# Performance work log

Hardware: AMD Instinct MI355X
Metric: run time of the kernel (lower is better)

The kernel has to match this reference:

```python
import jax, jax.numpy as jnp
import numpy as np

T = 200000  # stack depth
V = 130     # vocab_size == input_dim
H = 512     # hid_dim
L = 2       # n_layers


def setup_inputs() -> dict:
    key = jax.random.key(0)
    ks = jax.random.split(key, 24)
    s = 0.05
    inp = {
        "input": jax.random.normal(ks[0], (1, 1, V), jnp.float32),
        "prev_Val": jax.random.normal(ks[1], (T, V), jnp.float32),
        "prev_stg": jax.random.uniform(ks[2], (T,), jnp.float32),
        "prev_read": jax.random.normal(ks[3], (V,), jnp.float32),
        "prev_h": jax.random.normal(ks[4], (L, 1, H), jnp.float32) * 0.1,
        "prev_c": jax.random.normal(ks[5], (L, 1, H), jnp.float32) * 0.1,
        # LSTM layer 0 (pytorch layout: W_ih (4H, in), W_hh (4H, H), gates i,f,g,o)
        "W_ih0": jax.random.normal(ks[6], (4 * H, V), jnp.float32) * s,
        "W_hh0": jax.random.normal(ks[7], (4 * H, H), jnp.float32) * s,
        "b_ih0": jax.random.normal(ks[8], (4 * H,), jnp.float32) * s,
        "b_hh0": jax.random.normal(ks[9], (4 * H,), jnp.float32) * s,
        # LSTM layer 1
        "W_ih1": jax.random.normal(ks[10], (4 * H, H), jnp.float32) * s,
        "W_hh1": jax.random.normal(ks[11], (4 * H, H), jnp.float32) * s,
        "b_ih1": jax.random.normal(ks[12], (4 * H,), jnp.float32) * s,
        "b_hh1": jax.random.normal(ks[13], (4 * H,), jnp.float32) * s,
        # gate heads (original inits these to zeros; random here to exercise math)
        "Wd": jax.random.normal(ks[14], (H,), jnp.float32) * s,
        "Bd": jax.random.normal(ks[15], (), jnp.float32) * s,
        "Wu": jax.random.normal(ks[16], (H,), jnp.float32) * s,
        "Bu": jax.random.normal(ks[17], (), jnp.float32) * s,
        "Wv": jax.random.normal(ks[18], (H, V), jnp.float32) * s,
        "Bv": jax.random.normal(ks[19], (V,), jnp.float32) * s,
        "Wo": jax.random.normal(ks[20], (H, H), jnp.float32) * s,
        "Bo": jax.random.normal(ks[21], (H,), jnp.float32) * s,
    }
    return inp


def _lstm_cell(x, h, c, Wih, Whh, bih, bhh):
    # x: (1, in), h/c: (1, H)
    g = x @ Wih.T + h @ Whh.T + bih + bhh  # (1, 4H)
    i, f, gg, o = jnp.split(g, 4, axis=-1)
    c2 = jax.nn.sigmoid(f) * c + jax.nn.sigmoid(i) * jnp.tanh(gg)
    h2 = jax.nn.sigmoid(o) * jnp.tanh(c2)
    return h2, c2


def reference(input, prev_Val, prev_stg, prev_read, prev_h, prev_c,
              W_ih0, W_hh0, b_ih0, b_hh0, W_ih1, W_hh1, b_ih1, b_hh1,
              Wd, Bd, Wu, Bu, Wv, Bv, Wo, Bo):
    x = (input + prev_read)[0]  # (1, V), seq_len == 1, batch == 1
    h1, c1 = _lstm_cell(x, prev_h[0], prev_c[0], W_ih0, W_hh0, b_ih0, b_hh0)
    h2, c2 = _lstm_cell(h1, prev_h[1], prev_c[1], W_ih1, W_hh1, b_ih1, b_hh1)
    output = h2  # (1, H)

    dt = jax.nn.sigmoid(output @ Wd + Bd)[0]      # scalar push strength
    ut = jax.nn.sigmoid(output @ Wu + Bu)[0]      # scalar pop strength
    vt = jnp.tanh(output @ Wv + Bv)               # (1, V) pushed value
    ot = jnp.tanh(output @ Wo + Bo)               # (1, H) controller output

    Val = jnp.concatenate([prev_Val, vt], axis=0)  # (T+1, V)

    # pop pass (top -> bottom): stg[i] = max(0, prev_stg[i] - max(0, ut)); ut -= stg[i]
    def pop_step(u, s):
        sn = jnp.maximum(0.0, s - jnp.maximum(0.0, u))
        return u - sn, sn
    _, stg_popped = jax.lax.scan(pop_step, ut, prev_stg, reverse=True)
    stg = jnp.concatenate([stg_popped, dt[None]])  # (T+1,)

    # read pass (top -> bottom): coef = min(stg[i], max(0, read)); read -= stg[i]
    def read_step(r, s):
        coef = jnp.minimum(s, jnp.maximum(0.0, r))
        return r - s, coef
    _, coefs = jax.lax.scan(read_step, jnp.asarray(1.0, stg.dtype), stg, reverse=True)
    rt = coefs @ Val  # (V,)

    h_new = jnp.stack([h1, h2])  # (L, 1, H)
    c_new = jnp.stack([c1, c2])
    return ot, Val, stg, rt, h_new, c_new
```

## Files before the change

kernel.cpp:

```cpp
#include <hip/hip_runtime.h>

#define T_DEPTH 200000
#define V_DIM   130
#define H_DIM   512

#define OT_OFF   0
#define VAL_OFF  512
#define STG_OFF  26000642
#define RT_OFF   26200643
#define HN_OFF   26200773
#define CN_OFF   26201797

#define NV4 6500000
#define NS2 100000
#define A1  1625000
#define A2  3250000
#define A3  4875000
#define MVB 128
#define CPB 1536

typedef float f32x4 __attribute__((ext_vector_type(4)));
typedef float f32x2 __attribute__((ext_vector_type(2)));

static __device__ __forceinline__ float sigmoidf_(float x) {
  return 1.0f / (1.0f + expf(-x));
}

static __device__ __forceinline__ void copy_val4(const f32x4* __restrict__ vin,
                                                 f32x4* __restrict__ vout,
                                                 int lo, int hi, int w, int S) {
  int u = lo + w;
  for (; u + 3 * S < hi; u += 4 * S) {
    f32x4 a = __builtin_nontemporal_load(vin + u);
    f32x4 b = __builtin_nontemporal_load(vin + u + S);
    f32x4 c = __builtin_nontemporal_load(vin + u + 2 * S);
    f32x4 d = __builtin_nontemporal_load(vin + u + 3 * S);
    __builtin_nontemporal_store(a, vout + u);
    __builtin_nontemporal_store(b, vout + u + S);
    __builtin_nontemporal_store(c, vout + u + 2 * S);
    __builtin_nontemporal_store(d, vout + u + 3 * S);
  }
  for (; u < hi; u += S) {
    f32x4 a = __builtin_nontemporal_load(vin + u);
    __builtin_nontemporal_store(a, vout + u);
  }
}

static __device__ __forceinline__ void lstm_unit(
    const float* __restrict__ Wih, int in_dim,
    const float* __restrict__ x_a, const float* __restrict__ x_b,
    const float* __restrict__ Whh, const float* __restrict__ hprev,
    const float* __restrict__ bih, const float* __restrict__ bhh,
    const float* __restrict__ cprev, int j, int lane,
    float* __restrict__ h_out, float* __restrict__ c_out) {
  float pg[4];
#pragma unroll
  for (int q = 0; q < 4; ++q) {
    int row = q * H_DIM + j;
    const float* wr = Wih + row * in_dim;
    const float* wh = Whh + row * H_DIM;
    float acc = 0.f;
    if (x_b) {
      for (int c = lane; c < in_dim; c += 64) acc += wr[c] * (x_a[c] + x_b[c]);
    } else {
      for (int c = lane; c < in_dim; c += 64) acc += wr[c] * x_a[c];
    }
    for (int k = lane; k < H_DIM; k += 64) acc += wh[k] * hprev[k];
    for (int off = 32; off; off >>= 1) acc += __shfl_down(acc, off, 64);
    pg[q] = acc;
  }
  if (lane == 0) {
    float ig = sigmoidf_(pg[0] + bih[j] + bhh[j]);
    float fg = sigmoidf_(pg[1] + bih[H_DIM + j] + bhh[H_DIM + j]);
    float gg = tanhf(pg[2] + bih[2 * H_DIM + j] + bhh[2 * H_DIM + j]);
    float og = sigmoidf_(pg[3] + bih[3 * H_DIM + j] + bhh[3 * H_DIM + j]);
    float cn = fg * cprev[j] + ig * gg;
    float hn = og * tanhf(cn);
    h_out[j] = hn;
    c_out[j] = cn;
  }
}

__global__ void k1_l0(const float* __restrict__ Wih, const float* __restrict__ Whh,
                      const float* __restrict__ bih, const float* __restrict__ bhh,
                      const float* __restrict__ inp, const float* __restrict__ prd,
                      const float* __restrict__ hprev, const float* __restrict__ cprev,
                      const f32x4* __restrict__ vin, const f32x2* __restrict__ sin2,
                      float* __restrict__ out) {
  int bid = blockIdx.x, tid = threadIdx.x;
  if (bid < MVB) {
    lstm_unit(Wih, V_DIM, inp, prd, Whh, hprev, bih, bhh, cprev,
              bid * 4 + (tid >> 6), tid & 63, out + HN_OFF, out + CN_OFF);
  } else {
    int w = (bid - MVB) * 256 + tid;
    int S = (gridDim.x - MVB) * 256;
    f32x2* __restrict__ sout = reinterpret_cast<f32x2*>(out + STG_OFF);
    for (int u = w; u < NS2; u += S) {
      f32x2 sv = __builtin_nontemporal_load(sin2 + u);
      __builtin_nontemporal_store(sv, sout + u);
    }
    copy_val4(vin, reinterpret_cast<f32x4*>(out + VAL_OFF), 0, A1, w, S);
  }
}

__global__ void k2_l1(const float* __restrict__ Wih, const float* __restrict__ Whh,
                      const float* __restrict__ bih, const float* __restrict__ bhh,
                      const float* __restrict__ hprev, const float* __restrict__ cprev,
                      const f32x4* __restrict__ vin, float* __restrict__ out) {
  int bid = blockIdx.x, tid = threadIdx.x;
  if (bid < MVB) {
    lstm_unit(Wih, H_DIM, out + HN_OFF, nullptr, Whh, hprev, bih, bhh, cprev,
              bid * 4 + (tid >> 6), tid & 63,
              out + HN_OFF + H_DIM, out + CN_OFF + H_DIM);
  } else {
    int w = (bid - MVB) * 256 + tid;
    int S = (gridDim.x - MVB) * 256;
    copy_val4(vin, reinterpret_cast<f32x4*>(out + VAL_OFF), A1, A2, w, S);
  }
}

__global__ void k3_heads(const float* __restrict__ Wv, const float* __restrict__ Bv,
                         const float* __restrict__ Wo, const float* __restrict__ Bo,
                         const float* __restrict__ Wd, const float* __restrict__ Bd,
                         const float* __restrict__ Wu, const float* __restrict__ Bu,
                         const f32x4* __restrict__ vin, float* __restrict__ ws,
                         float* __restrict__ out) {
  int bid = blockIdx.x, tid = threadIdx.x;
  const float* h2 = out + HN_OFF + H_DIM;
  if (bid < 2) {
    int t = bid * 256 + tid;
    float a0 = 0.f, a1 = 0.f, a2 = 0.f, a3 = 0.f;
    for (int k = 0; k < H_DIM; k += 4) {
      a0 += h2[k]     * Wo[k * H_DIM + t];
      a1 += h2[k + 1] * Wo[(k + 1) * H_DIM + t];
      a2 += h2[k + 2] * Wo[(k + 2) * H_DIM + t];
      a3 += h2[k + 3] * Wo[(k + 3) * H_DIM + t];
    }
    out[OT_OFF + t] = tanhf(((a0 + a1) + (a2 + a3)) + Bo[t]);
  } else if (bid == 2) {
    if (tid < V_DIM) {
      float a0 = 0.f, a1 = 0.f, a2 = 0.f, a3 = 0.f;
      for (int k = 0; k < H_DIM; k += 4) {
        a0 += h2[k]     * Wv[k * V_DIM + tid];
        a1 += h2[k + 1] * Wv[(k + 1) * V_DIM + tid];
        a2 += h2[k + 2] * Wv[(k + 2) * V_DIM + tid];
        a3 += h2[k + 3] * Wv[(k + 3) * V_DIM + tid];
      }
      out[VAL_OFF + T_DEPTH * V_DIM + tid] = tanhf(((a0 + a1) + (a2 + a3)) + Bv[tid]);
    }
  } else if (bid == 3) {
    int wid = tid >> 6, lane = tid & 63;
    if (wid < 2) {
      const float* wv = (wid == 0) ? Wd : Wu;
      float acc = 0.f;
      for (int k = lane; k < H_DIM; k += 64) acc += h2[k] * wv[k];
      for (int off = 32; off; off >>= 1) acc += __shfl_down(acc, off, 64);
      if (lane == 0) {
        if (wid == 0) {
          float dt = sigmoidf_(acc + Bd[0]);
          ws[0] = dt;
          out[STG_OFF + T_DEPTH] = dt;
        } else {
          ws[1] = sigmoidf_(acc + Bu[0]);
        }
      }
    }
  } else {
    int w = (bid - 4) * 256 + tid;
    int S = (gridDim.x - 4) * 256;
    copy_val4(vin, reinterpret_cast<f32x4*>(out + VAL_OFF), A2, A3, w, S);
  }
}

__global__ void k4_top(const float* __restrict__ prev_stg, const float* __restrict__ prev_val,
                       const float* __restrict__ ws, const f32x4* __restrict__ vin,
                       float* __restrict__ out) {
  int bid = blockIdx.x, t = threadIdx.x;
  if (bid == 0) {
    float dt = ws[0];
    float u  = ws[1];
    float r  = 1.0f;
    float acc = 0.f;
    {
      float coef = fminf(dt, fmaxf(0.f, r));
      if (t < V_DIM) acc += coef * out[VAL_OFF + T_DEPTH * V_DIM + t];
      r -= dt;
    }
    for (int i = T_DEPTH - 1; i >= 0; --i) {
      bool pop_active = (u > 0.f);
      if (!pop_active && r <= 0.f) break;
      float s  = prev_stg[i];
      float sn = fmaxf(0.f, s - fmaxf(0.f, u));
      u -= sn;
      if (pop_active && t == 0) out[STG_OFF + i] = sn;
      float coef = fminf(sn, fmaxf(0.f, r));
      r -= sn;
      if (coef > 0.f && t < V_DIM) acc += coef * prev_val[i * V_DIM + t];
    }
    if (t < V_DIM) out[RT_OFF + t] = acc;
  } else {
    int w = (bid - 1) * 256 + t;
    int S = (gridDim.x - 1) * 256;
    copy_val4(vin, reinterpret_cast<f32x4*>(out + VAL_OFF), A3, NV4, w, S);
  }
}

extern "C" void kernel_launch(void* const* d_in, const int* in_sizes, int n_in,
                              void* d_out, int out_size, void* d_ws, size_t ws_size,
                              hipStream_t stream) {
  (void)in_sizes; (void)n_in; (void)out_size; (void)ws_size;
  const float* input     = (const float*)d_in[0];
  const float* prev_Val  = (const float*)d_in[1];
  const float* prev_stg  = (const float*)d_in[2];
  const float* prev_read = (const float*)d_in[3];
  const float* prev_h    = (const float*)d_in[4];
  const float* prev_c    = (const float*)d_in[5];
  const float* W_ih0 = (const float*)d_in[6];
  const float* W_hh0 = (const float*)d_in[7];
  const float* b_ih0 = (const float*)d_in[8];
  const float* b_hh0 = (const float*)d_in[9];
  const float* W_ih1 = (const float*)d_in[10];
  const float* W_hh1 = (const float*)d_in[11];
  const float* b_ih1 = (const float*)d_in[12];
  const float* b_hh1 = (const float*)d_in[13];
  const float* Wd = (const float*)d_in[14];
  const float* Bd = (const float*)d_in[15];
  const float* Wu = (const float*)d_in[16];
  const float* Bu = (const float*)d_in[17];
  const float* Wv = (const float*)d_in[18];
  const float* Bv = (const float*)d_in[19];
  const float* Wo = (const float*)d_in[20];
  const float* Bo = (const float*)d_in[21];

  float* out = (float*)d_out;
  float* ws  = (float*)d_ws;

  const f32x4* vin = (const f32x4*)prev_Val;
  const f32x2* sin2 = (const f32x2*)prev_stg;

  k1_l0<<<MVB + CPB, 256, 0, stream>>>(W_ih0, W_hh0, b_ih0, b_hh0, input, prev_read,
                                       prev_h, prev_c, vin, sin2, out);
  k2_l1<<<MVB + CPB, 256, 0, stream>>>(W_ih1, W_hh1, b_ih1, b_hh1,
                                       prev_h + H_DIM, prev_c + H_DIM, vin, out);
  k3_heads<<<4 + CPB, 256, 0, stream>>>(Wv, Bv, Wo, Bo, Wd, Bd, Wu, Bu, vin, ws, out);
  k4_top<<<1 + CPB, 256, 0, stream>>>(prev_stg, prev_Val, ws, vin, out);
}
```

Before: 297.2 us.

## Split bulk Val/stg copy into separate kernel ahead of serial LSTM chain

The large Val/stg copy is no longer spread across four kernels alongside the LSTM, head and stack work. It now runs as one dedicated grid-stride kernel with plain (temporal) loads and stores, followed by small LSTM, head and stack-pass kernels. Intermediate h and c now go to workspace instead of being read back from the output buffer. This removes the interleaving of the serial compute chain with the copy, but the small kernels no longer overlap with the copy, and the nontemporal hints are dropped.

```diff
diff --git a/kernel.cpp b/kernel.cpp
--- a/kernel.cpp
+++ b/kernel.cpp
@@ -11,38 +11,29 @@
 #define HN_OFF   26200773
 #define CN_OFF   26201797
 
+#define WS_DTUT  0
+#define WS_H1    64
+#define WS_C1    576
+#define WS_H2    1088
+#define WS_C2    1600
+
 #define NV4 6500000
 #define NS2 100000
-#define A1  1625000
-#define A2  3250000
-#define A3  4875000
-#define MVB 128
-#define CPB 1536
-
-typedef float f32x4 __attribute__((ext_vector_type(4)));
-typedef float f32x2 __attribute__((ext_vector_type(2)));
 
 static __device__ __forceinline__ float sigmoidf_(float x) {
   return 1.0f / (1.0f + expf(-x));
 }
 
-static __device__ __forceinline__ void copy_val4(const f32x4* __restrict__ vin,
-                                                 f32x4* __restrict__ vout,
-                                                 int lo, int hi, int w, int S) {
-  int u = lo + w;
-  for (; u + 3 * S < hi; u += 4 * S) {
-    f32x4 a = __builtin_nontemporal_load(vin + u);
-    f32x4 b = __builtin_nontemporal_load(vin + u + S);
-    f32x4 c = __builtin_nontemporal_load(vin + u + 2 * S);
-    f32x4 d = __builtin_nontemporal_load(vin + u + 3 * S);
-    __builtin_nontemporal_store(a, vout + u);
-    __builtin_nontemporal_store(b, vout + u + S);
-    __builtin_nontemporal_store(c, vout + u + 2 * S);
-    __builtin_nontemporal_store(d, vout + u + 3 * S);
-  }
-  for (; u < hi; u += S) {
-    f32x4 a = __builtin_nontemporal_load(vin + u);
-    __builtin_nontemporal_store(a, vout + u);
+__global__ void k_bulk(const float4* __restrict__ val_in,
+                       const float2* __restrict__ stg_in,
+                       float* __restrict__ out) {
+  const int NT = NV4 + NS2;
+  float4* __restrict__ val_out = reinterpret_cast<float4*>(out + VAL_OFF);
+  float2* __restrict__ stg_out = reinterpret_cast<float2*>(out + STG_OFF);
+  int stride = gridDim.x * blockDim.x;
+  for (int u = blockIdx.x * blockDim.x + threadIdx.x; u < NT; u += stride) {
+    if (u < NV4) val_out[u] = val_in[u];
+    else { int s = u - NV4; stg_out[s] = stg_in[s]; }
   }
 }
 
@@ -52,6 +43,7 @@
     const float* __restrict__ Whh, const float* __restrict__ hprev,
     const float* __restrict__ bih, const float* __restrict__ bhh,
     const float* __restrict__ cprev, int j, int lane,
+    float* __restrict__ h_ws, float* __restrict__ c_ws,
     float* __restrict__ h_out, float* __restrict__ c_out) {
   float pg[4];
 #pragma unroll
@@ -76,57 +68,37 @@
     float og = sigmoidf_(pg[3] + bih[3 * H_DIM + j] + bhh[3 * H_DIM + j]);
     float cn = fg * cprev[j] + ig * gg;
     float hn = og * tanhf(cn);
-    h_out[j] = hn;
-    c_out[j] = cn;
-  }
-}
-
-__global__ void k1_l0(const float* __restrict__ Wih, const float* __restrict__ Whh,
-                      const float* __restrict__ bih, const float* __restrict__ bhh,
-                      const float* __restrict__ inp, const float* __restrict__ prd,
-                      const float* __restrict__ hprev, const float* __restrict__ cprev,
-                      const f32x4* __restrict__ vin, const f32x2* __restrict__ sin2,
-                      float* __restrict__ out) {
+    h_ws[j] = hn; c_ws[j] = cn;
+    h_out[j] = hn; c_out[j] = cn;
+  }
+}
+
+__global__ void kL0(const float* __restrict__ Wih, const float* __restrict__ Whh,
+                    const float* __restrict__ bih, const float* __restrict__ bhh,
+                    const float* __restrict__ inp, const float* __restrict__ prd,
+                    const float* __restrict__ hprev, const float* __restrict__ cprev,
+                    float* __restrict__ ws, float* __restrict__ out) {
+  int j = blockIdx.x * 4 + (threadIdx.x >> 6), lane = threadIdx.x & 63;
+  lstm_unit(Wih, V_DIM, inp, prd, Whh, hprev, bih, bhh, cprev, j, lane,
+            ws + WS_H1, ws + WS_C1, out + HN_OFF, out + CN_OFF);
+}
+
+__global__ void kL1(const float* __restrict__ Wih, const float* __restrict__ Whh,
+                    const float* __restrict__ bih, const float* __restrict__ bhh,
+                    const float* __restrict__ hprev, const float* __restrict__ cprev,
+                    float* __restrict__ ws, float* __restrict__ out) {
+  int j = blockIdx.x * 4 + (threadIdx.x >> 6), lane = threadIdx.x & 63;
+  lstm_unit(Wih, H_DIM, ws + WS_H1, nullptr, Whh, hprev, bih, bhh, cprev, j, lane,
+            ws + WS_H2, ws + WS_C2, out + HN_OFF + H_DIM, out + CN_OFF + H_DIM);
+}
+
+__global__ void kheads(const float* __restrict__ Wv, const float* __restrict__ Bv,
+                       const float* __restrict__ Wo, const float* __restrict__ Bo,
+                       const float* __restrict__ Wd, const float* __restrict__ Bd,
+                       const float* __restrict__ Wu, const float* __restrict__ Bu,
+                       float* __restrict__ ws, float* __restrict__ out) {
   int bid = blockIdx.x, tid = threadIdx.x;
-  if (bid < MVB) {
-    lstm_unit(Wih, V_DIM, inp, prd, Whh, hprev, bih, bhh, cprev,
-              bid * 4 + (tid >> 6), tid & 63, out + HN_OFF, out + CN_OFF);
-  } else {
-    int w = (bid - MVB) * 256 + tid;
-    int S = (gridDim.x - MVB) * 256;
-    f32x2* __restrict__ sout = reinterpret_cast<f32x2*>(out + STG_OFF);
-    for (int u = w; u < NS2; u += S) {
-      f32x2 sv = __builtin_nontemporal_load(sin2 + u);
-      __builtin_nontemporal_store(sv, sout + u);
-    }
-    copy_val4(vin, reinterpret_cast<f32x4*>(out + VAL_OFF), 0, A1, w, S);
-  }
-}
-
-__global__ void k2_l1(const float* __restrict__ Wih, const float* __restrict__ Whh,
-                      const float* __restrict__ bih, const float* __restrict__ bhh,
-                      const float* __restrict__ hprev, const float* __restrict__ cprev,
-                      const f32x4* __restrict__ vin, float* __restrict__ out) {
-  int bid = blockIdx.x, tid = threadIdx.x;
-  if (bid < MVB) {
-    lstm_unit(Wih, H_DIM, out + HN_OFF, nullptr, Whh, hprev, bih, bhh, cprev,
-              bid * 4 + (tid >> 6), tid & 63,
-              out + HN_OFF + H_DIM, out + CN_OFF + H_DIM);
-  } else {
-    int w = (bid - MVB) * 256 + tid;
-    int S = (gridDim.x - MVB) * 256;
-    copy_val4(vin, reinterpret_cast<f32x4*>(out + VAL_OFF), A1, A2, w, S);
-  }
-}
-
-__global__ void k3_heads(const float* __restrict__ Wv, const float* __restrict__ Bv,
-                         const float* __restrict__ Wo, const float* __restrict__ Bo,
-                         const float* __restrict__ Wd, const float* __restrict__ Bd,
-                         const float* __restrict__ Wu, const float* __restrict__ Bu,
-                         const f32x4* __restrict__ vin, float* __restrict__ ws,
-                         float* __restrict__ out) {
-  int bid = blockIdx.x, tid = threadIdx.x;
-  const float* h2 = out + HN_OFF + H_DIM;
+  const float* h2 = ws + WS_H2;
   if (bid < 2) {
     int t = bid * 256 + tid;
     float a0 = 0.f, a1 = 0.f, a2 = 0.f, a3 = 0.f;
@@ -148,7 +120,7 @@
       }
       out[VAL_OFF + T_DEPTH * V_DIM + tid] = tanhf(((a0 + a1) + (a2 + a3)) + Bv[tid]);
     }
-  } else if (bid == 3) {
+  } else {
     int wid = tid >> 6, lane = tid & 63;
     if (wid < 2) {
       const float* wv = (wid == 0) ? Wd : Wu;
@@ -158,51 +130,40 @@
       if (lane == 0) {
         if (wid == 0) {
           float dt = sigmoidf_(acc + Bd[0]);
-          ws[0] = dt;
+          ws[WS_DTUT + 0] = dt;
           out[STG_OFF + T_DEPTH] = dt;
         } else {
-          ws[1] = sigmoidf_(acc + Bu[0]);
+          ws[WS_DTUT + 1] = sigmoidf_(acc + Bu[0]);
         }
       }
     }
-  } else {
-    int w = (bid - 4) * 256 + tid;
-    int S = (gridDim.x - 4) * 256;
-    copy_val4(vin, reinterpret_cast<f32x4*>(out + VAL_OFF), A2, A3, w, S);
-  }
-}
-
-__global__ void k4_top(const float* __restrict__ prev_stg, const float* __restrict__ prev_val,
-                       const float* __restrict__ ws, const f32x4* __restrict__ vin,
-                       float* __restrict__ out) {
-  int bid = blockIdx.x, t = threadIdx.x;
-  if (bid == 0) {
-    float dt = ws[0];
-    float u  = ws[1];
-    float r  = 1.0f;
-    float acc = 0.f;
-    {
-      float coef = fminf(dt, fmaxf(0.f, r));
-      if (t < V_DIM) acc += coef * out[VAL_OFF + T_DEPTH * V_DIM + t];
-      r -= dt;
-    }
-    for (int i = T_DEPTH - 1; i >= 0; --i) {
-      bool pop_active = (u > 0.f);
-      if (!pop_active && r <= 0.f) break;
-      float s  = prev_stg[i];
-      float sn = fmaxf(0.f, s - fmaxf(0.f, u));
-      u -= sn;
-      if (pop_active && t == 0) out[STG_OFF + i] = sn;
-      float coef = fminf(sn, fmaxf(0.f, r));
-      r -= sn;
-      if (coef > 0.f && t < V_DIM) acc += coef * prev_val[i * V_DIM + t];
-    }
-    if (t < V_DIM) out[RT_OFF + t] = acc;
-  } else {
-    int w = (bid - 1) * 256 + t;
-    int S = (gridDim.x - 1) * 256;
-    copy_val4(vin, reinterpret_cast<f32x4*>(out + VAL_OFF), A3, NV4, w, S);
-  }
+  }
+}
+
+__global__ void ktop(const float* __restrict__ prev_stg, const float* __restrict__ prev_val,
+                     const float* __restrict__ ws, float* __restrict__ out) {
+  int t = threadIdx.x;
+  float dt = ws[WS_DTUT + 0];
+  float u  = ws[WS_DTUT + 1];
+  float r  = 1.0f;
+  float acc = 0.f;
+  {
+    float coef = fminf(dt, fmaxf(0.f, r));
+    if (t < V_DIM) acc += coef * out[VAL_OFF + T_DEPTH * V_DIM + t];
+    r -= dt;
+  }
+  for (int i = T_DEPTH - 1; i >= 0; --i) {
+    bool pop_active = (u > 0.f);
+    if (!pop_active && r <= 0.f) break;
+    float s  = prev_stg[i];
+    float sn = fmaxf(0.f, s - fmaxf(0.f, u));
+    u -= sn;
+    if (pop_active && t == 0) out[STG_OFF + i] = sn;
+    float coef = fminf(sn, fmaxf(0.f, r));
+    r -= sn;
+    if (coef > 0.f && t < V_DIM) acc += coef * prev_val[i * V_DIM + t];
+  }
+  if (t < V_DIM) out[RT_OFF + t] = acc;
 }
 
 extern "C" void kernel_launch(void* const* d_in, const int* in_sizes, int n_in,
@@ -235,13 +196,11 @@
   float* out = (float*)d_out;
   float* ws  = (float*)d_ws;
 
-  const f32x4* vin = (const f32x4*)prev_Val;
-  const f32x2* sin2 = (const f32x2*)prev_stg;
-
-  k1_l0<<<MVB + CPB, 256, 0, stream>>>(W_ih0, W_hh0, b_ih0, b_hh0, input, prev_read,
-                                       prev_h, prev_c, vin, sin2, out);
-  k2_l1<<<MVB + CPB, 256, 0, stream>>>(W_ih1, W_hh1, b_ih1, b_hh1,
-                                       prev_h + H_DIM, prev_c + H_DIM, vin, out);
-  k3_heads<<<4 + CPB, 256, 0, stream>>>(Wv, Bv, Wo, Bo, Wd, Bd, Wu, Bu, vin, ws, out);
-  k4_top<<<1 + CPB, 256, 0, stream>>>(prev_stg, prev_Val, ws, vin, out);
-}
+  k_bulk<<<4096, 256, 0, stream>>>((const float4*)prev_Val, (const float2*)prev_stg, out);
+  kL0<<<128, 256, 0, stream>>>(W_ih0, W_hh0, b_ih0, b_hh0, input, prev_read,
+                               prev_h, prev_c, ws, out);
+  kL1<<<128, 256, 0, stream>>>(W_ih1, W_hh1, b_ih1, b_hh1,
+                               prev_h + H_DIM, prev_c + H_DIM, ws, out);
+  kheads<<<4, 256, 0, stream>>>(Wv, Bv, Wo, Bo, Wd, Bd, Wu, Bu, ws, out);
+  ktop<<<1, 192, 0, stream>>>(prev_stg, prev_Val, ws, out);
+}
```

Result: slower. 307.9 us (+3.6%).
